# Performance work log

Measured on AMD Instinct MI355X. Metric: run time of the kernel, lower is better.

Reference implementation:

```python
import jax, jax.numpy as jnp
import numpy as np

R = 4096          # proposals per image
D = 4096          # fc7 feature dim (VGG16)
C = 20            # foreground classes (VOC); logits have C+1 with background
IMG_W, IMG_H = 1216.0, 800.0
SCORE_THRESH = 0.05
NMS_THRESH = 0.5
TOPK = 100


def setup_inputs() -> dict:
    key = jax.random.key(0)
    k1, k2, k3, k4, k5 = jax.random.split(key, 5)
    x = jax.random.normal(k1, (R, D), dtype=jnp.float32)
    # build valid xyxy boxes inside the image
    xy = jax.random.uniform(k2, (R, 2)) * jnp.array([IMG_W * 0.8, IMG_H * 0.8])
    wh = jax.random.uniform(k3, (R, 2)) * jnp.array([IMG_W * 0.4, IMG_H * 0.4]) + 8.0
    boxes = jnp.concatenate([xy, xy + wh], axis=1).astype(jnp.float32)
    W_cls = (jax.random.normal(k4, (D, C + 1)) * 0.01).astype(jnp.float32)
    W_det = (jax.random.normal(k5, (D, C + 1)) * 0.01).astype(jnp.float32)
    b_cls = jnp.zeros((C + 1,), jnp.float32)
    b_det = jnp.zeros((C + 1,), jnp.float32)
    return {"x": x, "boxes": boxes, "W_cls": W_cls, "b_cls": b_cls,
            "W_det": W_det, "b_det": b_det}


def _iou_matrix(b):
    # b: (R, 4) xyxy -> (R, R) IoU
    area = (b[:, 2] - b[:, 0]) * (b[:, 3] - b[:, 1])
    lt = jnp.maximum(b[:, None, :2], b[None, :, :2])
    rb = jnp.minimum(b[:, None, 2:], b[None, :, 2:])
    wh = jnp.clip(rb - lt, 0.0)
    inter = wh[..., 0] * wh[..., 1]
    return inter / (area[:, None] + area[None, :] - inter + 1e-9)


def _nms_per_class(sc, iou):
    # sc: (R,) scores for one class; iou: (R, R) shared IoU matrix.
    # Sequential greedy NMS over score-descending order; returns bool keep mask.
    n = sc.shape[0]
    order = jnp.argsort(-sc)

    def step(supp, oi):
        kept = (sc[oi] > SCORE_THRESH) & jnp.logical_not(supp[oi])
        supp = jnp.where(kept, supp | (iou[oi] > NMS_THRESH), supp)
        return supp, kept

    _, keep_sorted = jax.lax.scan(step, jnp.zeros((n,), bool), order)
    return jnp.zeros((n,), bool).at[order].set(keep_sorted)


def reference(x, boxes, W_cls, b_cls, W_det, b_det):
    # WSDDN two-stream head: class softmax x proposal softmax
    cls_logits = x @ W_cls + b_cls                      # (R, C+1)
    det_logits = x @ W_det + b_det                      # (R, C+1)
    scores = jax.nn.softmax(cls_logits, axis=1) * jax.nn.softmax(det_logits, axis=0)
    scores = scores[:, :-1]                             # drop background column (R, C)

    # clip boxes to image (Boxes.clip)
    b = jnp.stack([jnp.clip(boxes[:, 0], 0.0, IMG_W),
                   jnp.clip(boxes[:, 1], 0.0, IMG_H),
                   jnp.clip(boxes[:, 2], 0.0, IMG_W),
                   jnp.clip(boxes[:, 3], 0.0, IMG_H)], axis=1)

    iou = _iou_matrix(b)                                # (R, R)
    # per-class NMS (batched_nms with class-agnostic boxes == independent per-class NMS)
    keep = jax.vmap(lambda s: _nms_per_class(s, iou), in_axes=1, out_axes=1)(scores)  # (R, C)

    kept_scores = scores * keep.astype(scores.dtype)
    flat = kept_scores.reshape(-1)                      # (R*C,)
    top_vals, top_idx = jax.lax.top_k(flat, TOPK)
    top_prop = top_idx // C
    top_cls = top_idx % C
    top_boxes = b[top_prop]                             # (TOPK, 4)
    return top_vals, top_boxes, top_cls
```

## Files before the change

kernel.cpp:

```cpp
#include <hip/hip_runtime.h>
#include <math.h>

#define R_N 4096
#define D_N 4096
#define C_N 20
#define IMG_W_F 1216.0f
#define IMG_H_F 800.0f
#define SCORE_TH 0.05f
#define NMS_TH 0.5f
#define TOPK_N 100

#define WF_WORDS   (128 * 2 * 64 * 4)
#define CTRL_OFF   (WF_WORDS)
#define CAND_R_OFF (CTRL_OFF + 64)
#define CAND_D_OFF (CAND_R_OFF + 640)

typedef short bf16x8 __attribute__((ext_vector_type(8)));
typedef float f32x4  __attribute__((ext_vector_type(4)));

__device__ __forceinline__ unsigned pk(float a, float b) {
  return __builtin_amdgcn_perm(__float_as_uint(a), __float_as_uint(b), 0x07060302u);
}
__device__ __forceinline__ float fexp(float x) { return __expf(x); }

__device__ __forceinline__ void load_clip_box(const float* boxes, int r, float* b) {
  b[0] = fminf(fmaxf(boxes[r * 4 + 0], 0.f), IMG_W_F);
  b[1] = fminf(fmaxf(boxes[r * 4 + 1], 0.f), IMG_H_F);
  b[2] = fminf(fmaxf(boxes[r * 4 + 2], 0.f), IMG_W_F);
  b[3] = fminf(fmaxf(boxes[r * 4 + 3], 0.f), IMG_H_F);
}

__global__ __launch_bounds__(256) void wT_kernel(
    const float* __restrict__ Wd, uint4* __restrict__ Wfrag,
    int* __restrict__ ctrl) {
  const int e = blockIdx.x * 256 + threadIdx.x;
  const int l = e & 63;
  const int ct = (e >> 6) & 1;
  const int gs = e >> 7;
  const int c = ct * 16 + (l & 15);
  const int k0 = gs * 32 + (l >> 4) * 8;
  float w[8];
  if (c < 21) {
#pragma unroll
    for (int j = 0; j < 8; j++) w[j] = Wd[(size_t)(k0 + j) * 21 + c];
  } else {
#pragma unroll
    for (int j = 0; j < 8; j++) w[j] = 0.f;
  }
  uint4 v;
  v.x = pk(w[1], w[0]); v.y = pk(w[3], w[2]);
  v.z = pk(w[5], w[4]); v.w = pk(w[7], w[6]);
  Wfrag[(gs * 2 + ct) * 64 + l] = v;
  if (e < 42) ctrl[e] = 0;
}

__global__ __launch_bounds__(1024) void detgemm_kernel(
    const float* __restrict__ x, const uint4* __restrict__ Wfrag,
    float* __restrict__ dsum, int* __restrict__ nc,
    int* __restrict__ done1, int* __restrict__ done2,
    int* __restrict__ cand_r, float* __restrict__ cand_d,
    const float* __restrict__ Wc, const float* __restrict__ b_cls,
    const float* __restrict__ boxes, float* __restrict__ out) {
  __shared__ float red[16 * 512];
  __shared__ float ex[320];
  __shared__ float sd[20];
  __shared__ int   snc[20];
  __shared__ int   s_last, s_total;

  const int t = threadIdx.x;
  const int w = t >> 6, l = t & 63;
  const int r16 = l & 15, q = l >> 4;
  const int r0 = blockIdx.x * 16;

  const float* xrow = x + (size_t)(r0 + r16) * D_N + w * 256 + q * 8;
  float4 a[16];
#pragma unroll
  for (int s = 0; s < 8; s++) {
    a[2 * s]     = *(const float4*)(xrow + s * 32);
    a[2 * s + 1] = *(const float4*)(xrow + s * 32 + 4);
  }

  f32x4 acc0 = {0.f, 0.f, 0.f, 0.f};
  f32x4 acc1 = {0.f, 0.f, 0.f, 0.f};
#pragma unroll
  for (int s = 0; s < 8; s++) {
    const int gs = w * 8 + s;
    union { uint4 u; bf16x8 v; } b0, b1;
    b0.u = Wfrag[(gs * 2 + 0) * 64 + l];
    b1.u = Wfrag[(gs * 2 + 1) * 64 + l];
    union { bf16x8 v; unsigned u[4]; } af;
    af.u[0] = pk(a[2 * s].y,     a[2 * s].x);
    af.u[1] = pk(a[2 * s].w,     a[2 * s].z);
    af.u[2] = pk(a[2 * s + 1].y, a[2 * s + 1].x);
    af.u[3] = pk(a[2 * s + 1].w, a[2 * s + 1].z);
    acc0 = __builtin_amdgcn_mfma_f32_16x16x32_bf16(af.v, b0.v, acc0, 0, 0, 0);
    acc1 = __builtin_amdgcn_mfma_f32_16x16x32_bf16(af.v, b1.v, acc1, 0, 0, 0);
  }

  *(f32x4*)(&red[w * 512 + (0  + r16) * 16 + q * 4]) = acc0;
  *(f32x4*)(&red[w * 512 + (16 + r16) * 16 + q * 4]) = acc1;
  __syncthreads();
  if (t < 512) {
    float v = 0.f;
#pragma unroll
    for (int w2 = 0; w2 < 16; w2++) v += red[w2 * 512 + t];
    red[t] = v;
  }
  __syncthreads();
  if (t < 320) ex[t] = fexp(red[t]);
  __syncthreads();
  if (t < 20) {
    float s = 0.f;
#pragma unroll
    for (int r = 0; r < 16; r++) s += ex[t * 16 + r];
    atomicAdd(&dsum[t], s);
  }
  __syncthreads();

  if (t == 0) {
    atomicAdd(done1, 1);
    while (atomicAdd(done1, 0) < 256) __builtin_amdgcn_s_sleep(8);
  }
  __syncthreads();
  if (t < 20) sd[t] = atomicAdd(&dsum[t], 0.0f);
  __syncthreads();

  if (t < 320) {
    const int c = t >> 4, r = t & 15;
    float dsm = ex[t] / sd[c];
    if (dsm > SCORE_TH) {
      int p = atomicAdd(&nc[c], 1);
      if (p < 32) {
        atomicExch(&cand_r[c * 32 + p], r0 + r);
        atomicExch(&cand_d[c * 32 + p], dsm);
      }
    }
  }
  __syncthreads();
  if (t == 0) s_last = (atomicAdd(done2, 1) == 255) ? 1 : 0;
  __syncthreads();
  if (!s_last) return;

  if (t < 20) snc[t] = atomicAdd(&nc[t], 0);
  __syncthreads();
  if (t == 0) {
    int tot = 0;
#pragma unroll
    for (int c = 0; c < 20; c++) tot += (snc[c] > 32 ? 32 : snc[c]);
    s_total = tot;
  }
  __syncthreads();

  if (s_total == 0) {
    if (t < TOPK_N) {
      int prop = t / C_N;
      int cls = t - prop * C_N;
      float b[4]; load_clip_box(boxes, prop, b);
      out[t] = 0.f;
      out[TOPK_N + t * 4 + 0] = b[0];
      out[TOPK_N + t * 4 + 1] = b[1];
      out[TOPK_N + t * 4 + 2] = b[2];
      out[TOPK_N + t * 4 + 3] = b[3];
      out[TOPK_N * 5 + t] = (float)cls;
    }
    return;
  }

  float* cand_s = red;
  int*   s_ki   = (int*)(red + 640);
  float* s_ks   = red + 1152;
  float* sval   = red + 1664;
  int*   sidx   = (int*)(red + 1764);
  int*   s_kc   = (int*)(red + 1864);

  if (t == 0) *s_kc = 0;
  if (t < TOPK_N) { sval[t] = 0.f; sidx[t] = 0; }
  __syncthreads();

  for (int slot = t; slot < 640; slot += 1024) {
    const int c = slot >> 5, i = slot & 31;
    int n = snc[c]; if (n > 32) n = 32;
    if (i < n) {
      const int rr = atomicAdd(&cand_r[slot], 0);
      float lg[21];
#pragma unroll
      for (int j = 0; j < 21; j++) lg[j] = b_cls[j];
      const float* xr = x + (size_t)rr * D_N;
      for (int k = 0; k < D_N; k++) {
        float xv = xr[k];
        const float* wr = Wc + (size_t)k * 21;
#pragma unroll
        for (int j = 0; j < 21; j++) lg[j] = fmaf(xv, wr[j], lg[j]);
      }
      float m = -1e30f;
#pragma unroll
      for (int j = 0; j < 21; j++) m = fmaxf(m, lg[j]);
      float s = 0.f;
#pragma unroll
      for (int j = 0; j < 21; j++) s += fexp(lg[j] - m);
      float p = fexp(lg[c] - m) / s;
      cand_s[slot] = p * atomicAdd(&cand_d[slot], 0.0f);
    }
  }
  __syncthreads();

  if (t < 20) {
    const int c = t;
    int n = snc[c]; if (n > 32) n = 32;
    float s[32]; int rr[32]; int n2 = 0;
    for (int i = 0; i < n; i++) {
      float sc = cand_s[c * 32 + i];
      if (sc > SCORE_TH) { s[n2] = sc; rr[n2] = atomicAdd(&cand_r[c * 32 + i], 0); n2++; }
    }
    for (int i = 1; i < n2; i++) {
      float si = s[i]; int ri = rr[i];
      int j = i - 1;
      while (j >= 0 && (s[j] < si || (s[j] == si && rr[j] > ri))) {
        s[j + 1] = s[j]; rr[j + 1] = rr[j]; j--;
      }
      s[j + 1] = si; rr[j + 1] = ri;
    }
    unsigned supp = 0;
    for (int i = 0; i < n2; i++) {
      if (supp & (1u << i)) continue;
      int g = atomicAdd(s_kc, 1);
      if (g < 512) { s_ki[g] = rr[i] * C_N + c; s_ks[g] = s[i]; }
      float bi[4]; load_clip_box(boxes, rr[i], bi);
      float ai = (bi[2] - bi[0]) * (bi[3] - bi[1]);
      for (int j = i + 1; j < n2; j++) {
        if (supp & (1u << j)) continue;
        float bj[4]; load_clip_box(boxes, rr[j], bj);
        float aj = (bj[2] - bj[0]) * (bj[3] - bj[1]);
        float lx = fmaxf(bi[0], bj[0]), ly = fmaxf(bi[1], bj[1]);
        float rx = fminf(bi[2], bj[2]), ry = fminf(bi[3], bj[3]);
        float wdt = fmaxf(rx - lx, 0.f), hgt = fmaxf(ry - ly, 0.f);
        float inter = wdt * hgt;
        float iou = inter / (ai + aj - inter + 1e-9f);
        if (iou > NMS_TH) supp |= (1u << j);
      }
    }
  }
  __syncthreads();

  int m = *s_kc; if (m > 512) m = 512;
  for (int i = t; i < m; i += 1024) {
    float si = s_ks[i]; int xi = s_ki[i];
    int rank = 0;
    for (int j = 0; j < m; j++) {
      float sj = s_ks[j]; int xj = s_ki[j];
      if (sj > si || (sj == si && xj < xi)) rank++;
    }
    if (rank < TOPK_N) { sval[rank] = si; sidx[rank] = xi; }
  }
  __syncthreads();
  if (t == 0) {
    int f = m < TOPK_N ? m : TOPK_N;
    int cur = 0;
    for (int slot = f; slot < TOPK_N; slot++) {
      for (;;) {
        bool member = false;
        for (int j = 0; j < m; j++)
          if (s_ki[j] == cur) { member = true; break; }
        if (!member) break;
        cur++;
      }
      sval[slot] = 0.f;
      sidx[slot] = cur;
      cur++;
    }
  }
  __syncthreads();
  if (t < TOPK_N) {
    int idx = sidx[t];
    int prop = idx / C_N;
    int cls = idx - prop * C_N;
    float b[4]; load_clip_box(boxes, prop, b);
    out[t] = sval[t];
    out[TOPK_N + t * 4 + 0] = b[0];
    out[TOPK_N + t * 4 + 1] = b[1];
    out[TOPK_N + t * 4 + 2] = b[2];
    out[TOPK_N + t * 4 + 3] = b[3];
    out[TOPK_N * 5 + t] = (float)cls;
  }
}

extern "C" void kernel_launch(void* const* d_in, const int* in_sizes, int n_in,
                              void* d_out, int out_size, void* d_ws, size_t ws_size,
                              hipStream_t stream) {
  const float* x     = (const float*)d_in[0];
  const float* boxes = (const float*)d_in[1];
  const float* W_cls = (const float*)d_in[2];
  const float* b_cls = (const float*)d_in[3];
  const float* W_det = (const float*)d_in[4];

  float* out = (float*)d_out;
  float* ws = (float*)d_ws;
  uint4* Wfrag  = (uint4*)ws;
  float* dsum   = ws + CTRL_OFF;
  int*   nc     = (int*)(ws + CTRL_OFF) + 20;
  int*   done1  = (int*)(ws + CTRL_OFF) + 40;
  int*   done2  = (int*)(ws + CTRL_OFF) + 41;
  int*   cand_r = (int*)(ws + CAND_R_OFF);
  float* cand_d = ws + CAND_D_OFF;

  wT_kernel     <<<64,  256,  0, stream>>>(W_det, Wfrag, (int*)(ws + CTRL_OFF));
  detgemm_kernel<<<256, 1024, 0, stream>>>(x, Wfrag, dsum, nc, done1, done2,
                                           cand_r, cand_d, W_cls, b_cls, boxes, out);
}
```

Baseline: 120.3 us.

## Split det GEMM over K into 512 blocks and move softmax/NMS to separate scan kernel

The det-logit GEMM is split along K into two halves, doubling the block count to 512. Each block writes its partial logits transposed to a workspace buffer instead of doing the softmax and grid barrier itself. A new 32-block scan kernel sums the two partials, computes the column softmax and candidate selection with a smaller grid-wide spin barrier, and runs the final NMS/top-k. This is meant to spread the x read across more CUs and cut the cost of a 256-block spin barrier, at the price of an extra launch and a partial-logit round trip through global memory.

```diff
diff --git a/kernel.cpp b/kernel.cpp
--- a/kernel.cpp
+++ b/kernel.cpp
@@ -12,7 +12,9 @@
 
 #define WF_WORDS   (128 * 2 * 64 * 4)
 #define CTRL_OFF   (WF_WORDS)
-#define CAND_R_OFF (CTRL_OFF + 64)
+#define DETT_OFF   (CTRL_OFF + 64)
+#define DETT_WORDS (2 * 20 * R_N)
+#define CAND_R_OFF (DETT_OFF + DETT_WORDS)
 #define CAND_D_OFF (CAND_R_OFF + 640)
 
 typedef short bf16x8 __attribute__((ext_vector_type(8)));
@@ -30,10 +32,10 @@
   b[3] = fminf(fmaxf(boxes[r * 4 + 3], 0.f), IMG_H_F);
 }
 
-__global__ __launch_bounds__(256) void wT_kernel(
+__global__ __launch_bounds__(128) void wT_kernel(
     const float* __restrict__ Wd, uint4* __restrict__ Wfrag,
     int* __restrict__ ctrl) {
-  const int e = blockIdx.x * 256 + threadIdx.x;
+  const int e = blockIdx.x * 128 + threadIdx.x;
   const int l = e & 63;
   const int ct = (e >> 6) & 1;
   const int gs = e >> 7;
@@ -51,40 +53,35 @@
   v.x = pk(w[1], w[0]); v.y = pk(w[3], w[2]);
   v.z = pk(w[5], w[4]); v.w = pk(w[7], w[6]);
   Wfrag[(gs * 2 + ct) * 64 + l] = v;
-  if (e < 42) ctrl[e] = 0;
+  if (e < 64) ctrl[e] = 0;
 }
 
 __global__ __launch_bounds__(1024) void detgemm_kernel(
     const float* __restrict__ x, const uint4* __restrict__ Wfrag,
-    float* __restrict__ dsum, int* __restrict__ nc,
-    int* __restrict__ done1, int* __restrict__ done2,
-    int* __restrict__ cand_r, float* __restrict__ cand_d,
-    const float* __restrict__ Wc, const float* __restrict__ b_cls,
-    const float* __restrict__ boxes, float* __restrict__ out) {
+    float* __restrict__ detT) {
   __shared__ float red[16 * 512];
-  __shared__ float ex[320];
-  __shared__ float sd[20];
-  __shared__ int   snc[20];
-  __shared__ int   s_last, s_total;
-
   const int t = threadIdx.x;
   const int w = t >> 6, l = t & 63;
   const int r16 = l & 15, q = l >> 4;
-  const int r0 = blockIdx.x * 16;
-
-  const float* xrow = x + (size_t)(r0 + r16) * D_N + w * 256 + q * 8;
-  float4 a[16];
-#pragma unroll
-  for (int s = 0; s < 8; s++) {
+  const int rblk = blockIdx.x >> 1;
+  const int kb   = blockIdx.x & 1;
+  const int r0 = rblk * 16;
+
+  const float* xrow = x + (size_t)(r0 + r16) * D_N + kb * 2048 + w * 128 + q * 8;
+
+  float4 a[8];
+#pragma unroll
+  for (int s = 0; s < 4; s++) {
     a[2 * s]     = *(const float4*)(xrow + s * 32);
     a[2 * s + 1] = *(const float4*)(xrow + s * 32 + 4);
   }
+  __builtin_amdgcn_sched_barrier(0);
 
   f32x4 acc0 = {0.f, 0.f, 0.f, 0.f};
   f32x4 acc1 = {0.f, 0.f, 0.f, 0.f};
 #pragma unroll
-  for (int s = 0; s < 8; s++) {
-    const int gs = w * 8 + s;
+  for (int s = 0; s < 4; s++) {
+    const int gs = kb * 64 + w * 4 + s;
     union { uint4 u; bf16x8 v; } b0, b1;
     b0.u = Wfrag[(gs * 2 + 0) * 64 + l];
     b1.u = Wfrag[(gs * 2 + 1) * 64 + l];
@@ -107,41 +104,69 @@
     red[t] = v;
   }
   __syncthreads();
-  if (t < 320) ex[t] = fexp(red[t]);
+  if (t < 320) {
+    const int c = t >> 4, r = t & 15;
+    detT[(size_t)(kb * 20 + c) * R_N + r0 + r] = red[t];
+  }
+}
+
+__global__ __launch_bounds__(1024) void scan_kernel(
+    const float* __restrict__ x, const float* __restrict__ Wc,
+    const float* __restrict__ b_cls, const float* __restrict__ detT,
+    float* __restrict__ dsum, int* __restrict__ nc,
+    int* __restrict__ done1, int* __restrict__ done2,
+    int* __restrict__ cand_r, float* __restrict__ cand_d,
+    const float* __restrict__ boxes, float* __restrict__ out) {
+  __shared__ float sm[2560];
+  __shared__ float sd[20];
+  __shared__ int   snc[20];
+  __shared__ int   s_last, s_total;
+  const int t = threadIdx.x;
+  const int rbase = blockIdx.x * 128;
+
+  for (int idx = t; idx < 2560; idx += 1024) {
+    const int c = idx >> 7, r = idx & 127;
+    float lg = detT[(size_t)c * R_N + rbase + r] +
+               detT[(size_t)(20 + c) * R_N + rbase + r];
+    sm[idx] = fexp(lg);
+  }
   __syncthreads();
   if (t < 20) {
     float s = 0.f;
 #pragma unroll
-    for (int r = 0; r < 16; r++) s += ex[t * 16 + r];
+    for (int r = 0; r < 128; r++) s += sm[t * 128 + r];
     atomicAdd(&dsum[t], s);
   }
   __syncthreads();
 
   if (t == 0) {
-    atomicAdd(done1, 1);
-    while (atomicAdd(done1, 0) < 256) __builtin_amdgcn_s_sleep(8);
-  }
-  __syncthreads();
-  if (t < 20) sd[t] = atomicAdd(&dsum[t], 0.0f);
-  __syncthreads();
-
-  if (t < 320) {
-    const int c = t >> 4, r = t & 15;
-    float dsm = ex[t] / sd[c];
+    __hip_atomic_fetch_add(done1, 1, __ATOMIC_RELEASE, __HIP_MEMORY_SCOPE_AGENT);
+    while (__hip_atomic_load(done1, __ATOMIC_ACQUIRE, __HIP_MEMORY_SCOPE_AGENT) < 32)
+      __builtin_amdgcn_s_sleep(2);
+  }
+  __syncthreads();
+  if (t < 20) sd[t] = __hip_atomic_load(&dsum[t], __ATOMIC_RELAXED, __HIP_MEMORY_SCOPE_AGENT);
+  __syncthreads();
+
+  for (int idx = t; idx < 2560; idx += 1024) {
+    const int c = idx >> 7, r = idx & 127;
+    float dsm = sm[idx] / sd[c];
     if (dsm > SCORE_TH) {
       int p = atomicAdd(&nc[c], 1);
       if (p < 32) {
-        atomicExch(&cand_r[c * 32 + p], r0 + r);
+        atomicExch(&cand_r[c * 32 + p], rbase + r);
         atomicExch(&cand_d[c * 32 + p], dsm);
       }
     }
   }
   __syncthreads();
-  if (t == 0) s_last = (atomicAdd(done2, 1) == 255) ? 1 : 0;
+  if (t == 0)
+    s_last = (__hip_atomic_fetch_add(done2, 1, __ATOMIC_ACQ_REL, __HIP_MEMORY_SCOPE_AGENT) == 31)
+               ? 1 : 0;
   __syncthreads();
   if (!s_last) return;
 
-  if (t < 20) snc[t] = atomicAdd(&nc[t], 0);
+  if (t < 20) snc[t] = __hip_atomic_load(&nc[t], __ATOMIC_RELAXED, __HIP_MEMORY_SCOPE_AGENT);
   __syncthreads();
   if (t == 0) {
     int tot = 0;
@@ -166,12 +191,12 @@
     return;
   }
 
-  float* cand_s = red;
-  int*   s_ki   = (int*)(red + 640);
-  float* s_ks   = red + 1152;
-  float* sval   = red + 1664;
-  int*   sidx   = (int*)(red + 1764);
-  int*   s_kc   = (int*)(red + 1864);
+  float* cand_s = sm;
+  int*   s_ki   = (int*)(sm + 640);
+  float* s_ks   = sm + 1152;
+  float* sval   = sm + 1664;
+  int*   sidx   = (int*)(sm + 1764);
+  int*   s_kc   = (int*)(sm + 1864);
 
   if (t == 0) *s_kc = 0;
   if (t < TOPK_N) { sval[t] = 0.f; sidx[t] = 0; }
@@ -181,7 +206,7 @@
     const int c = slot >> 5, i = slot & 31;
     int n = snc[c]; if (n > 32) n = 32;
     if (i < n) {
-      const int rr = atomicAdd(&cand_r[slot], 0);
+      const int rr = __hip_atomic_load(&cand_r[slot], __ATOMIC_RELAXED, __HIP_MEMORY_SCOPE_AGENT);
       float lg[21];
 #pragma unroll
       for (int j = 0; j < 21; j++) lg[j] = b_cls[j];
@@ -199,7 +224,8 @@
 #pragma unroll
       for (int j = 0; j < 21; j++) s += fexp(lg[j] - m);
       float p = fexp(lg[c] - m) / s;
-      cand_s[slot] = p * atomicAdd(&cand_d[slot], 0.0f);
+      float dv = __hip_atomic_load(&cand_d[slot], __ATOMIC_RELAXED, __HIP_MEMORY_SCOPE_AGENT);
+      cand_s[slot] = p * dv;
     }
   }
   __syncthreads();
@@ -210,7 +236,11 @@
     float s[32]; int rr[32]; int n2 = 0;
     for (int i = 0; i < n; i++) {
       float sc = cand_s[c * 32 + i];
-      if (sc > SCORE_TH) { s[n2] = sc; rr[n2] = atomicAdd(&cand_r[c * 32 + i], 0); n2++; }
+      if (sc > SCORE_TH) {
+        s[n2] = sc;
+        rr[n2] = __hip_atomic_load(&cand_r[c * 32 + i], __ATOMIC_RELAXED, __HIP_MEMORY_SCOPE_AGENT);
+        n2++;
+      }
     }
     for (int i = 1; i < n2; i++) {
       float si = s[i]; int ri = rr[i];
@@ -300,10 +330,12 @@
   int*   nc     = (int*)(ws + CTRL_OFF) + 20;
   int*   done1  = (int*)(ws + CTRL_OFF) + 40;
   int*   done2  = (int*)(ws + CTRL_OFF) + 41;
+  float* detT   = ws + DETT_OFF;
   int*   cand_r = (int*)(ws + CAND_R_OFF);
   float* cand_d = ws + CAND_D_OFF;
 
-  wT_kernel     <<<64,  256,  0, stream>>>(W_det, Wfrag, (int*)(ws + CTRL_OFF));
-  detgemm_kernel<<<256, 1024, 0, stream>>>(x, Wfrag, dsum, nc, done1, done2,
-                                           cand_r, cand_d, W_cls, b_cls, boxes, out);
-}
+  wT_kernel     <<<128, 128,  0, stream>>>(W_det, Wfrag, (int*)(ws + CTRL_OFF));
+  detgemm_kernel<<<512, 1024, 0, stream>>>(x, Wfrag, detT);
+  scan_kernel   <<<32,  1024, 0, stream>>>(x, W_cls, b_cls, detT, dsum, nc,
+                                           done1, done2, cand_r, cand_d, boxes, out);
+}
```

New measurement: 114.3 us. 5.0% less time.
